# Optimization experiments

Hardware: AMD Instinct MI355X
Metric: run time of the kernel (lower is better)

## Reference

```python
import jax, jax.numpy as jnp
import numpy as np


def _compute_shifts(num_patches, multiplier=1, stride=1):
    """Replicates the Python loop's shift schedule, including the sticky `inv`
    variable bug (inv starts as False==0, becomes -1 permanently after the first
    (w_idx%3==1, h_idx%3==1) entry with w_idx != h_idx)."""
    shifts = np.zeros(num_patches, dtype=np.int32)
    inv_state = 0  # Python `inv` starts as False
    m = multiplier * stride
    for i in range(num_patches):
        w_idx = i % 7  # hardcoded 7 in the original source
        h_idx = i // 7
        a, b = w_idx % 3, h_idx % 3
        if a == 0 and b == 0:
            s = -4 * m
        elif a == 0 and b == 1:
            s = m
        elif a == 0 and b == 2:
            s = 2 * m
        elif a == 1 and b == 0:
            s = -m
        elif a == 1 and b == 1:
            if w_idx != h_idx:
                inv_state = -1
            s = inv_state * m
        elif a == 1 and b == 2:
            s = 3 * m
        elif a == 2 and b == 0:
            s = -2 * m
        elif a == 2 and b == 1:
            s = -3 * m
        else:  # a == 2 and b == 2
            s = 4 * m
        shifts[i] = s
    return shifts


def setup_inputs() -> dict:
    key = jax.random.key(0)
    x = jax.random.normal(key, (16, 16, 14, 14, 768), dtype=jnp.float32)
    return {"x": x}


def reference(x):
    # x: [B, T, H, W, c]. With sx=sy=1 the random scatter fills the idx buffer
    # with all -1, so the stable argsort yields the identity permutation
    # shift_idx = arange(H*W). multiplier = 1 since inv=False.
    B, T, H, W, c = x.shape
    N = H * W
    shifts = jnp.asarray(_compute_shifts(N, multiplier=1, stride=1))  # [N]
    feat = x.reshape(B, T, N, c)
    # torch.roll(v, shifts=s, dims=time): out[t] = v[(t - s) % T]
    t_idx = (jnp.arange(T)[:, None] - shifts[None, :]) % T  # [T, N]
    out = feat[:, t_idx, jnp.arange(N)[None, :], :]  # [B, T, N, c] fused gather
    return out.reshape(B, T, H, W, c)
```

## Files before the change

kernel.cpp:

```cpp
#include <hip/hip_runtime.h>


typedef float f4 __attribute__((ext_vector_type(4)));

__global__ __launch_bounds__(192) void Rand2dPatchShift_kernel(
        const f4* __restrict__ x, f4* __restrict__ out) {
    const int n = blockIdx.x;
    const int b = blockIdx.y;

    const int w  = n % 7;
    const int h  = n / 7;
    const int a3 = w % 3;
    const int b3 = h % 3;

    int s;
    if (a3 == 0)      s = (b3 == 0) ? -4 : (b3 == 1 ? 1 : 2);
    else if (a3 == 1) s = (b3 == 0) ? -1 : (b3 == 1 ? ((n == 8) ? 0 : -1) : 3);
    else              s = (b3 == 0) ? -2 : (b3 == 1 ? -3 : 4);

    const long long base = ((long long)b * 16 * 196 + n) * 192 + threadIdx.x;
    const long long tstride = 196 * 192;

    f4 v[16];
#pragma unroll
    for (int t = 0; t < 16; ++t) {
        const int tsrc = (t - s + 16) & 15;
        v[t] = __builtin_nontemporal_load(&x[base + (long long)tsrc * tstride]);
    }
#pragma unroll
    for (int t = 0; t < 16; ++t) {
        __builtin_nontemporal_store(v[t], &out[base + (long long)t * tstride]);
    }
}

extern "C" void kernel_launch(void* const* d_in, const int* in_sizes, int n_in,
                              void* d_out, int out_size, void* d_ws, size_t ws_size,
                              hipStream_t stream) {
    const f4* x = (const f4*)d_in[0];
    f4* out = (f4*)d_out;

    dim3 grid(196, 16);
    dim3 block(192);
    Rand2dPatchShift_kernel<<<grid, block, 0, stream>>>(x, out);
}
```

Before: 251.3 us.

## Flatten gather into contiguous output tiles with per-element source index

Replaces the per-(patch,batch) block that gathered all 16 time steps with a flat 1D grid in which each 256-thread block writes a contiguous 2048-float4 output tile and computes each element's source index by integer division. Output writes become fully contiguous and the grid has more, smaller blocks. Loads switch from nontemporal to regular. The cost is extra integer div/mod arithmetic per element, and reads are scattered in shifted time slices.

Measured after the change: 262.2 us. +4.3%, slower.

```diff
diff --git a/kernel.cpp b/kernel.cpp
--- a/kernel.cpp
+++ b/kernel.cpp
@@ -3,34 +3,44 @@
 
 typedef float f4 __attribute__((ext_vector_type(4)));
 
-__global__ __launch_bounds__(192) void Rand2dPatchShift_kernel(
+#define TOTAL_F4 9633792u
+#define TILE_F4  2048u
+#define NBLOCKS  4704u
+
+__global__ __launch_bounds__(256) void Rand2dPatchShift_kernel(
         const f4* __restrict__ x, f4* __restrict__ out) {
-    const int n = blockIdx.x;
-    const int b = blockIdx.y;
+    const unsigned base = blockIdx.x * TILE_F4 + threadIdx.x;
 
-    const int w  = n % 7;
-    const int h  = n / 7;
-    const int a3 = w % 3;
-    const int b3 = h % 3;
+    unsigned srcIdx[8];
+#pragma unroll
+    for (int k = 0; k < 8; ++k) {
+        const unsigned idx  = base + (unsigned)k * 256u;
+        const unsigned lane = idx % 192u;
+        const unsigned r    = idx / 192u;
+        const unsigned n    = r % 196u;
+        const unsigned q    = r / 196u;
+        const unsigned t    = q & 15u;
+        const unsigned b    = q >> 4;
 
-    int s;
-    if (a3 == 0)      s = (b3 == 0) ? -4 : (b3 == 1 ? 1 : 2);
-    else if (a3 == 1) s = (b3 == 0) ? -1 : (b3 == 1 ? ((n == 8) ? 0 : -1) : 3);
-    else              s = (b3 == 0) ? -2 : (b3 == 1 ? -3 : 4);
+        const unsigned w  = n % 7u;
+        const unsigned h  = n / 7u;
+        const unsigned a3 = w % 3u;
+        const unsigned b3 = h % 3u;
+        int s;
+        if (a3 == 0u)      s = (b3 == 0u) ? -4 : (b3 == 1u ? 1 : 2);
+        else if (a3 == 1u) s = (b3 == 0u) ? -1 : (b3 == 1u ? ((n == 8u) ? 0 : -1) : 3);
+        else               s = (b3 == 0u) ? -2 : (b3 == 1u ? -3 : 4);
 
-    const long long base = ((long long)b * 16 * 196 + n) * 192 + threadIdx.x;
-    const long long tstride = 196 * 192;
+        const unsigned tsrc = (unsigned)(((int)t - s) & 15);
+        srcIdx[k] = ((b * 16u + tsrc) * 196u + n) * 192u + lane;
+    }
 
-    f4 v[16];
+    f4 v[8];
 #pragma unroll
-    for (int t = 0; t < 16; ++t) {
-        const int tsrc = (t - s + 16) & 15;
-        v[t] = __builtin_nontemporal_load(&x[base + (long long)tsrc * tstride]);
-    }
+    for (int k = 0; k < 8; ++k) v[k] = x[srcIdx[k]];
 #pragma unroll
-    for (int t = 0; t < 16; ++t) {
-        __builtin_nontemporal_store(v[t], &out[base + (long long)t * tstride]);
-    }
+    for (int k = 0; k < 8; ++k)
+        __builtin_nontemporal_store(v[k], &out[base + (unsigned)k * 256u]);
 }
 
 extern "C" void kernel_launch(void* const* d_in, const int* in_sizes, int n_in,
@@ -39,7 +49,5 @@
     const f4* x = (const f4*)d_in[0];
     f4* out = (f4*)d_out;
 
-    dim3 grid(196, 16);
-    dim3 block(192);
-    Rand2dPatchShift_kernel<<<grid, block, 0, stream>>>(x, out);
+    Rand2dPatchShift_kernel<<<dim3(NBLOCKS), dim3(256), 0, stream>>>(x, out);
 }
```
